# Kernel tuning notes

Hardware: AMD Instinct MI355X
Metric: run time of the kernel (lower is better)

Reference implementation:

```python
import jax, jax.numpy as jnp
import numpy as np

HEADS = 16
HEAD_DIM = 64
DIM = 1024
INNER = HEADS * HEAD_DIM
EPS = 1e-5


def setup_inputs() -> dict:
    key = jax.random.key(0)
    k_x, k_qkv, k_out, k_b = jax.random.split(key, 4)
    B, L = 2, 2048
    x = jax.random.normal(k_x, (B, L, DIM), dtype=jnp.float32)
    # Linear weights stored as [in, out] for x @ W
    w_qkv = jax.random.normal(k_qkv, (DIM, 3 * INNER), dtype=jnp.float32) * (DIM ** -0.5)
    w_out = jax.random.normal(k_out, (INNER, DIM), dtype=jnp.float32) * (INNER ** -0.5)
    b_out = jax.random.normal(k_b, (DIM,), dtype=jnp.float32) * 0.02
    gamma = jnp.ones((DIM,), dtype=jnp.float32)
    beta = jnp.zeros((DIM,), dtype=jnp.float32)
    return {"x": x, "w_qkv": w_qkv, "w_out": w_out, "b_out": b_out, "gamma": gamma, "beta": beta}


def reference(x, w_qkv, w_out, b_out, gamma, beta):
    B, L, C = x.shape
    scale = HEAD_DIM ** -0.5
    qkv = x @ w_qkv  # [B, L, 3*INNER]
    q, k, v = jnp.split(qkv, 3, axis=-1)
    # [B, L, INNER] -> [B, H, L, D]
    def split_heads(t):
        return t.reshape(B, L, HEADS, HEAD_DIM).transpose(0, 2, 1, 3)
    q, k, v = split_heads(q), split_heads(k), split_heads(v)
    dots = jnp.einsum('bhid,bhjd->bhij', q, k) * scale
    attn = jax.nn.softmax(dots, axis=-1)
    out = jnp.einsum('bhij,bhjd->bhid', attn, v)
    out = out.transpose(0, 2, 1, 3).reshape(B, L, INNER)
    out = out @ w_out + b_out
    res = x + out
    mean = jnp.mean(res, axis=-1, keepdims=True)
    var = jnp.var(res, axis=-1, keepdims=True)
    return (res - mean) * jax.lax.rsqrt(var + EPS) * gamma + beta
```

## Files before the change

kernel.cpp:

```cpp
#include <hip/hip_runtime.h>
#include <hip/hip_bf16.h>
#include <stdint.h>

#define HEADS 16
#define HDIM  64
#define DIMC  1024
#define INNER 1024
#define LSEQ  2048
#define BLM   4096

typedef unsigned short u16;
typedef __attribute__((ext_vector_type(8))) short bf16x8;
typedef __attribute__((ext_vector_type(4))) float f32x4;

__device__ __forceinline__ u16 f2bf(float f) {
  union { float f; uint32_t u; } v; v.f = f;
  uint32_t u = v.u;
  return (u16)((u + 0x7fffu + ((u >> 16) & 1u)) >> 16);
}
__device__ __forceinline__ uint32_t pack_bf2(float a, float b) {
  float2 f2; f2.x = a; f2.y = b;
  __hip_bfloat162 t = __float22bfloat162_rn(f2);
  union { __hip_bfloat162 h; uint32_t u; } c; c.h = t; return c.u;
}
__device__ __forceinline__ float fast_exp2(float x) {
  float r; asm("v_exp_f32 %0, %1" : "=v"(r) : "v"(x)); return r;
}

__device__ __forceinline__ void load_lds16(const void* g, void* l) {
  __builtin_amdgcn_global_load_lds(
      (const __attribute__((address_space(1))) uint32_t*)g,
      (__attribute__((address_space(3))) uint32_t*)l, 16, 0, 0);
}

__global__ __launch_bounds__(256) void prep_k(const float* __restrict__ x,
                                              const float* __restrict__ w_qkv,
                                              u16* __restrict__ xb,
                                              u16* __restrict__ wqkvT) {
  __shared__ float tile[32][33];
  int bid = blockIdx.x;
  if (bid < 4096) {
    int i = (bid * 256 + threadIdx.x) * 4;
    float4 v = *(const float4*)(x + i);
    ushort4 o;
    o.x = f2bf(v.x); o.y = f2bf(v.y); o.z = f2bf(v.z); o.w = f2bf(v.w);
    *(ushort4*)(xb + i) = o;
    return;
  }
  int idx = bid - 4096;
  int bx = idx % 96, by = idx / 96;
  int c0 = bx * 32, r0 = by * 32;
  int j = threadIdx.x & 31, i0 = threadIdx.x >> 5;
#pragma unroll
  for (int p = 0; p < 4; ++p) {
    int i = i0 + p * 8;
    tile[i][j] = w_qkv[(size_t)(r0 + i) * 3072 + (c0 + j)];
  }
  __syncthreads();
#pragma unroll
  for (int p = 0; p < 4; ++p) {
    int i = i0 + p * 8;
    wqkvT[(size_t)(c0 + i) * 1024 + (r0 + j)] = f2bf(tile[j][i]);
  }
}

__global__ __launch_bounds__(256) void transpose_cast_k(const float* __restrict__ in,
                                                        u16* __restrict__ out,
                                                        int R, int C) {
  __shared__ float tile[32][33];
  int c0 = blockIdx.x * 32, r0 = blockIdx.y * 32;
  int j = threadIdx.x & 31, i0 = threadIdx.x >> 5;
#pragma unroll
  for (int p = 0; p < 4; ++p) {
    int i = i0 + p * 8;
    tile[i][j] = in[(size_t)(r0 + i) * C + (c0 + j)];
  }
  __syncthreads();
#pragma unroll
  for (int p = 0; p < 4; ++p) {
    int i = i0 + p * 8;
    out[(size_t)(c0 + i) * R + (r0 + j)] = f2bf(tile[j][i]);
  }
}

template <int EPI, int TM>
__global__ __launch_bounds__(256) void gemm_bt(const u16* __restrict__ A,
                                               const u16* __restrict__ Bt,
                                               u16* __restrict__ Cb,
                                               float* __restrict__ Cf,
                                               const float* __restrict__ bias,
                                               const float* __restrict__ resid,
                                               u16* __restrict__ Vt,
                                               int M, int N, int K) {
  constexpr int MI = TM / 32;
  __shared__ alignas(16) u16 As[TM * 64];
  __shared__ alignas(16) u16 Bs[128 * 64];
  const int tid = threadIdx.x;
  const int lane = tid & 63;
  const int w = tid >> 6;
  const int wm = w >> 1, wn = w & 1;
  const int m0 = blockIdx.y * TM, n0 = blockIdx.x * 128;
  const int ln = lane & 15, qq = lane >> 4;
  const f32x4 zero4 = {0.f, 0.f, 0.f, 0.f};

  f32x4 acc[MI][4];
#pragma unroll
  for (int i = 0; i < MI; ++i)
#pragma unroll
    for (int j = 0; j < 4; ++j) acc[i][j] = zero4;

  for (int kt = 0; kt < K; kt += 64) {
    __syncthreads();
#pragma unroll
    for (int p = 0; p < TM / 32; ++p) {
      int t = p * 256 + tid;
      int r = t >> 3;
      int cl = (t & 7) ^ (r & 7);
      load_lds16(A + (size_t)(m0 + r) * K + kt + cl * 8,
                 (char*)As + (p * 256 + w * 64) * 16);
    }
#pragma unroll
    for (int p = 0; p < 4; ++p) {
      int t = p * 256 + tid;
      int r = t >> 3;
      int cl = (t & 7) ^ (r & 7);
      load_lds16(Bt + (size_t)(n0 + r) * K + kt + cl * 8,
                 (char*)Bs + (p * 256 + w * 64) * 16);
    }
    __syncthreads();
#pragma unroll
    for (int ks = 0; ks < 2; ++ks) {
      bf16x8 af[MI], bfr[4];
#pragma unroll
      for (int i = 0; i < MI; ++i) {
        int ra = wm * (TM / 2) + i * 16 + ln;
        af[i] = *(const bf16x8*)(As + (ra * 8 + ((ks * 4 + qq) ^ (ra & 7))) * 8);
      }
#pragma unroll
      for (int j = 0; j < 4; ++j) {
        int rb = wn * 64 + j * 16 + ln;
        bfr[j] = *(const bf16x8*)(Bs + (rb * 8 + ((ks * 4 + qq) ^ (rb & 7))) * 8);
      }
#pragma unroll
      for (int i = 0; i < MI; ++i)
#pragma unroll
        for (int j = 0; j < 4; ++j)
          acc[i][j] = __builtin_amdgcn_mfma_f32_16x16x32_bf16(af[i], bfr[j],
                                                              acc[i][j], 0, 0, 0);
    }
  }

#pragma unroll
  for (int i = 0; i < MI; ++i) {
#pragma unroll
    for (int j = 0; j < 4; ++j) {
      int col = n0 + wn * 64 + j * 16 + ln;
      if (EPI == 1) {
#pragma unroll
        for (int rr = 0; rr < 4; ++rr) {
          int row = m0 + wm * (TM / 2) + i * 16 + qq * 4 + rr;
          Cf[(size_t)row * N + col] =
              acc[i][j][rr] + bias[col] + resid[(size_t)row * N + col];
        }
      } else {
        if (col < 2048) {
#pragma unroll
          for (int rr = 0; rr < 4; ++rr) {
            int row = m0 + wm * (TM / 2) + i * 16 + qq * 4 + rr;
            Cb[(size_t)row * 2048 + col] = f2bf(acc[i][j][rr]);
          }
        } else {
          int dg = col - 2048;
          int hh = dg >> 6, dd = dg & 63;
          int l0 = (m0 & 2047) + wm * (TM / 2) + i * 16 + qq * 4;
          int bb = m0 >> 11;
          ushort4 pk;
          pk.x = f2bf(acc[i][j][0]); pk.y = f2bf(acc[i][j][1]);
          pk.z = f2bf(acc[i][j][2]); pk.w = f2bf(acc[i][j][3]);
          *(ushort4*)(Vt + (((size_t)bb * 16 + hh) * 64 + dd) * 2048 + l0) = pk;
        }
      }
    }
  }
}

__global__ __launch_bounds__(256) void attn_fused(const u16* __restrict__ qk,
                                                  const u16* __restrict__ vt,
                                                  u16* __restrict__ outp) {
  const int bh = blockIdx.x & 31;
  const int qt = blockIdx.x >> 5;
  const int h = bh & 15;
  const int b = bh >> 4;
  const int tid = threadIdx.x;
  const int lane = tid & 63;
  const int w = tid >> 6;
  const int ln = lane & 15, q4 = lane >> 4;
  const int l7 = ln & 7;
  const f32x4 zero4 = {0.f, 0.f, 0.f, 0.f};

  __shared__ alignas(16) u16 Ks[64 * 64];
  __shared__ alignas(16) u16 Vs[64 * 64];
  __shared__ alignas(16) u16 Ps[4][16 * 64];

  const size_t bh_tok = (size_t)b * LSEQ;
  const size_t vbase = ((size_t)b * 16 + h) * 64 * 2048;
  const int baseQ = h * HDIM;

  const float qscale = 0.125f * 1.44269504088896340736f;
  bf16x8 qf[2];
  {
    int row = qt * 64 + w * 16 + ln;
    const u16* p = qk + (bh_tok + row) * 2048 + baseQ;
#pragma unroll
    for (int ks = 0; ks < 2; ++ks) {
      bf16x8 v = *(const bf16x8*)(p + q4 * 8 + 32 * ks);
      bf16x8 o;
#pragma unroll
      for (int jj = 0; jj < 8; ++jj) {
        union { uint32_t u; float f; } cv; cv.u = ((uint32_t)(u16)v[jj]) << 16;
        o[jj] = (short)f2bf(cv.f * qscale);
      }
      qf[ks] = o;
    }
  }

  float lsum = 0.f;
  f32x4 o_acc[4];
#pragma unroll
  for (int dt = 0; dt < 4; ++dt) o_acc[dt] = zero4;

  u16* pw_base = &Ps[w][0];

  for (int jt = 0; jt < 32; ++jt) {
    const int key0 = jt * 64;
    __syncthreads();
#pragma unroll
    for (int iss = 0; iss < 2; ++iss) {
      int idx = iss * 256 + tid;
      int row = idx >> 3, c = idx & 7;
      int cl = c ^ (row & 7);
      load_lds16(qk + (bh_tok + key0 + row) * 2048 + 1024 + baseQ + cl * 8,
                 (char*)Ks + (iss * 256 + w * 64) * 16);
      load_lds16(vt + vbase + (size_t)row * 2048 + key0 + cl * 8,
                 (char*)Vs + (iss * 256 + w * 64) * 16);
    }
    __syncthreads();

    f32x4 S[4];
#pragma unroll
    for (int kt = 0; kt < 4; ++kt) {
      f32x4 a = zero4;
#pragma unroll
      for (int ks = 0; ks < 2; ++ks) {
        bf16x8 kf = *(const bf16x8*)(
            Ks + (((kt * 16 + ln) * 8 + ((ks * 4 + q4) ^ l7)) * 8));
        a = __builtin_amdgcn_mfma_f32_16x16x32_bf16(kf, qf[ks], a, 0, 0, 0);
      }
      S[kt] = a;
    }

#pragma unroll
    for (int kt = 0; kt < 4; ++kt)
#pragma unroll
      for (int r = 0; r < 4; ++r) {
        float p = fast_exp2(S[kt][r]);
        S[kt][r] = p;
        lsum += p;
      }

#pragma unroll
    for (int kt = 0; kt < 4; ++kt) {
      uint2 pd;
      pd.x = pack_bf2(S[kt][0], S[kt][1]);
      pd.y = pack_bf2(S[kt][2], S[kt][3]);
      int u = kt * 2 + (q4 >> 1);
      *(uint2*)(pw_base + ln * 64 + ((u ^ l7) * 8) + (q4 & 1) * 4) = pd;
    }
    asm volatile("s_waitcnt lgkmcnt(0)" ::: "memory");

    bf16x8 pf0 = *(const bf16x8*)(pw_base + ln * 64 + (((0 * 4 + q4) ^ l7) * 8));
    bf16x8 pf1 = *(const bf16x8*)(pw_base + ln * 64 + (((1 * 4 + q4) ^ l7) * 8));

#pragma unroll
    for (int dt = 0; dt < 4; ++dt) {
      bf16x8 va0 = *(const bf16x8*)(
          Vs + (((dt * 16 + ln) * 8 + ((0 * 4 + q4) ^ l7)) * 8));
      o_acc[dt] = __builtin_amdgcn_mfma_f32_16x16x32_bf16(va0, pf0, o_acc[dt], 0, 0, 0);
      bf16x8 va1 = *(const bf16x8*)(
          Vs + (((dt * 16 + ln) * 8 + ((1 * 4 + q4) ^ l7)) * 8));
      o_acc[dt] = __builtin_amdgcn_mfma_f32_16x16x32_bf16(va1, pf1, o_acc[dt], 0, 0, 0);
    }
  }

  lsum += __shfl_xor(lsum, 16);
  lsum += __shfl_xor(lsum, 32);
  float rl = 1.0f / lsum;

  asm volatile("s_waitcnt lgkmcnt(0)" ::: "memory");
#pragma unroll
  for (int dt = 0; dt < 4; ++dt) {
    uint2 pd;
    pd.x = pack_bf2(o_acc[dt][0] * rl, o_acc[dt][1] * rl);
    pd.y = pack_bf2(o_acc[dt][2] * rl, o_acc[dt][3] * rl);
    int u = dt * 2 + (q4 >> 1);
    *(uint2*)(pw_base + ln * 64 + ((u ^ l7) * 8) + (q4 & 1) * 4) = pd;
  }
  asm volatile("s_waitcnt lgkmcnt(0)" ::: "memory");
#pragma unroll
  for (int half = 0; half < 2; ++half) {
    int rr = half * 8 + (lane >> 3);
    int ch = lane & 7;
    bf16x8 rowv = *(const bf16x8*)(pw_base + rr * 64 + ((ch ^ (rr & 7)) * 8));
    int tok = qt * 64 + w * 16 + rr;
    *(bf16x8*)(outp + (bh_tok + tok) * 1024 + baseQ + ch * 8) = rowv;
  }
}

__global__ __launch_bounds__(256) void ln_k(const float* __restrict__ res,
                                            const float* __restrict__ gamma,
                                            const float* __restrict__ beta,
                                            float* __restrict__ out) {
  int w = threadIdx.x >> 6, lane = threadIdx.x & 63;
  int row = blockIdx.x * 4 + w;
  const float* r = res + (size_t)row * DIMC;
  float4 v[4];
  float s = 0.f, ss = 0.f;
#pragma unroll
  for (int p = 0; p < 4; ++p) {
    v[p] = *(const float4*)(r + (p * 64 + lane) * 4);
    s += v[p].x + v[p].y + v[p].z + v[p].w;
    ss += v[p].x * v[p].x + v[p].y * v[p].y + v[p].z * v[p].z + v[p].w * v[p].w;
  }
#pragma unroll
  for (int off = 1; off < 64; off <<= 1) {
    s += __shfl_xor(s, off);
    ss += __shfl_xor(ss, off);
  }
  float mean = s * (1.0f / DIMC);
  float var = ss * (1.0f / DIMC) - mean * mean;
  float inv = rsqrtf(var + 1e-5f);
#pragma unroll
  for (int p = 0; p < 4; ++p) {
    int c = (p * 64 + lane) * 4;
    float4 g = *(const float4*)(gamma + c);
    float4 bt = *(const float4*)(beta + c);
    float4 o;
    o.x = (v[p].x - mean) * inv * g.x + bt.x;
    o.y = (v[p].y - mean) * inv * g.y + bt.y;
    o.z = (v[p].z - mean) * inv * g.z + bt.z;
    o.w = (v[p].w - mean) * inv * g.w + bt.w;
    *(float4*)(out + (size_t)row * DIMC + c) = o;
  }
}

extern "C" void kernel_launch(void* const* d_in, const int* in_sizes, int n_in,
                              void* d_out, int out_size, void* d_ws, size_t ws_size,
                              hipStream_t stream) {
  const float* x = (const float*)d_in[0];
  const float* w_qkv = (const float*)d_in[1];
  const float* w_out = (const float*)d_in[2];
  const float* b_out = (const float*)d_in[3];
  const float* gamma = (const float*)d_in[4];
  const float* beta = (const float*)d_in[5];
  float* outp = (float*)d_out;
  char* ws = (char*)d_ws;

  u16* xb = (u16*)(ws);
  u16* wqkvT = (u16*)(ws + ((size_t)8 << 20));
  u16* qk = (u16*)(ws + ((size_t)14 << 20));
  u16* vt = (u16*)(ws + ((size_t)30 << 20));
  u16* attnout = (u16*)(ws);
  u16* woutT = (u16*)(ws + ((size_t)8 << 20));
  float* res = (float*)(ws + ((size_t)14 << 20));

  prep_k<<<7168, 256, 0, stream>>>(x, w_qkv, xb, wqkvT);
  gemm_bt<2, 128><<<dim3(24, 32), 256, 0, stream>>>(xb, wqkvT, qk, nullptr,
                                                    nullptr, nullptr, vt,
                                                    BLM, 3072, 1024);
  transpose_cast_k<<<dim3(32, 32), 256, 0, stream>>>(w_out, woutT, 1024, 1024);
  attn_fused<<<1024, 256, 0, stream>>>(qk, vt, attnout);
  gemm_bt<1, 64><<<dim3(8, 64), 256, 0, stream>>>(attnout, woutT, nullptr, res,
                                                  b_out, x, nullptr,
                                                  BLM, 1024, 1024);
  ln_k<<<1024, 256, 0, stream>>>(res, gamma, beta, outp);
}
```

Before: 206.2 us.

## Double-buffer K/V tiles and split attention waves over query and key halves

The attention kernel now double-buffers K and V tiles in shared memory, prefetching the next key tile while computing the current one, and uses a single barrier per iteration instead of two. Work is repartitioned so each wave handles 32 query rows against 32 keys of the tile, which reuses each K and V fragment across two query subtiles. The two key-half partial outputs and row sums are combined through shared memory at the end. This adds LDS use, register pressure and a final reduction step in exchange for overlapping global loads with MFMA work and cutting LDS fragment reads.

```diff
diff --git a/kernel.cpp b/kernel.cpp
--- a/kernel.cpp
+++ b/kernel.cpp
@@ -194,125 +194,197 @@
   const int tid = threadIdx.x;
   const int lane = tid & 63;
   const int w = tid >> 6;
+  const int wq = w & 1;
+  const int wk = w >> 1;
   const int ln = lane & 15, q4 = lane >> 4;
   const int l7 = ln & 7;
+  const int swz = (ln >> 1) & 3;
   const f32x4 zero4 = {0.f, 0.f, 0.f, 0.f};
 
-  __shared__ alignas(16) u16 Ks[64 * 64];
-  __shared__ alignas(16) u16 Vs[64 * 64];
-  __shared__ alignas(16) u16 Ps[4][16 * 64];
+  __shared__ alignas(16) char smem[40960];
+  u16* Ksb = (u16*)smem;
+  u16* Vsb = (u16*)(smem + 16384);
+  u16* Psw = (u16*)(smem + 32768);
 
   const size_t bh_tok = (size_t)b * LSEQ;
   const size_t vbase = ((size_t)b * 16 + h) * 64 * 2048;
   const int baseQ = h * HDIM;
 
+  bf16x8 qraw[2][2];
+#pragma unroll
+  for (int nt = 0; nt < 2; ++nt) {
+    int row = qt * 64 + wq * 32 + nt * 16 + ln;
+    const u16* p = qk + (bh_tok + row) * 2048 + baseQ;
+#pragma unroll
+    for (int ks = 0; ks < 2; ++ks)
+      qraw[nt][ks] = *(const bf16x8*)(p + q4 * 8 + 32 * ks);
+  }
+
+#pragma unroll
+  for (int iss = 0; iss < 2; ++iss) {
+    int idx = iss * 256 + tid;
+    int row = idx >> 3, c = idx & 7;
+    int cl = c ^ (row & 7);
+    load_lds16(qk + (bh_tok + row) * 2048 + 1024 + baseQ + cl * 8,
+               (char*)Ksb + (iss * 256 + w * 64) * 16);
+    load_lds16(vt + vbase + (size_t)row * 2048 + cl * 8,
+               (char*)Vsb + (iss * 256 + w * 64) * 16);
+  }
+
   const float qscale = 0.125f * 1.44269504088896340736f;
-  bf16x8 qf[2];
-  {
-    int row = qt * 64 + w * 16 + ln;
-    const u16* p = qk + (bh_tok + row) * 2048 + baseQ;
+  bf16x8 qf[2][2];
+#pragma unroll
+  for (int nt = 0; nt < 2; ++nt)
 #pragma unroll
     for (int ks = 0; ks < 2; ++ks) {
-      bf16x8 v = *(const bf16x8*)(p + q4 * 8 + 32 * ks);
+      bf16x8 v = qraw[nt][ks];
       bf16x8 o;
 #pragma unroll
       for (int jj = 0; jj < 8; ++jj) {
         union { uint32_t u; float f; } cv; cv.u = ((uint32_t)(u16)v[jj]) << 16;
         o[jj] = (short)f2bf(cv.f * qscale);
       }
-      qf[ks] = o;
-    }
-  }
-
-  float lsum = 0.f;
-  f32x4 o_acc[4];
-#pragma unroll
-  for (int dt = 0; dt < 4; ++dt) o_acc[dt] = zero4;
-
-  u16* pw_base = &Ps[w][0];
-
+      qf[nt][ks] = o;
+    }
+
+  float lsum[2] = {0.f, 0.f};
+  f32x4 o_acc[4][2];
+#pragma unroll
+  for (int dt = 0; dt < 4; ++dt) {
+    o_acc[dt][0] = zero4;
+    o_acc[dt][1] = zero4;
+  }
+
+  u16* pw = Psw + w * 1024;
+
+  asm volatile("s_waitcnt vmcnt(0)" ::: "memory");
+  __builtin_amdgcn_s_barrier();
+
+  int cur = 0;
+#pragma unroll 1
   for (int jt = 0; jt < 32; ++jt) {
-    const int key0 = jt * 64;
-    __syncthreads();
-#pragma unroll
-    for (int iss = 0; iss < 2; ++iss) {
-      int idx = iss * 256 + tid;
-      int row = idx >> 3, c = idx & 7;
-      int cl = c ^ (row & 7);
-      load_lds16(qk + (bh_tok + key0 + row) * 2048 + 1024 + baseQ + cl * 8,
-                 (char*)Ks + (iss * 256 + w * 64) * 16);
-      load_lds16(vt + vbase + (size_t)row * 2048 + key0 + cl * 8,
-                 (char*)Vs + (iss * 256 + w * 64) * 16);
-    }
-    __syncthreads();
-
-    f32x4 S[4];
-#pragma unroll
-    for (int kt = 0; kt < 4; ++kt) {
-      f32x4 a = zero4;
+    if (jt < 31) {
+      const int key0 = (jt + 1) * 64;
+#pragma unroll
+      for (int iss = 0; iss < 2; ++iss) {
+        int idx = iss * 256 + tid;
+        int row = idx >> 3, c = idx & 7;
+        int cl = c ^ (row & 7);
+        load_lds16(qk + (bh_tok + key0 + row) * 2048 + 1024 + baseQ + cl * 8,
+                   (char*)Ksb + (cur ^ 1) * 8192 + (iss * 256 + w * 64) * 16);
+        load_lds16(vt + vbase + (size_t)row * 2048 + key0 + cl * 8,
+                   (char*)Vsb + (cur ^ 1) * 8192 + (iss * 256 + w * 64) * 16);
+      }
+    }
+
+    const u16* Ks = Ksb + cur * 4096;
+    const u16* Vs = Vsb + cur * 4096;
+
+    f32x4 s_[2][2];
+#pragma unroll
+    for (int kt = 0; kt < 2; ++kt) { s_[kt][0] = zero4; s_[kt][1] = zero4; }
+#pragma unroll
+    for (int kt = 0; kt < 2; ++kt) {
+      int row = wk * 32 + kt * 16 + ln;
 #pragma unroll
       for (int ks = 0; ks < 2; ++ks) {
-        bf16x8 kf = *(const bf16x8*)(
-            Ks + (((kt * 16 + ln) * 8 + ((ks * 4 + q4) ^ l7)) * 8));
-        a = __builtin_amdgcn_mfma_f32_16x16x32_bf16(kf, qf[ks], a, 0, 0, 0);
-      }
-      S[kt] = a;
-    }
-
-#pragma unroll
-    for (int kt = 0; kt < 4; ++kt)
-#pragma unroll
-      for (int r = 0; r < 4; ++r) {
-        float p = fast_exp2(S[kt][r]);
-        S[kt][r] = p;
-        lsum += p;
-      }
-
-#pragma unroll
-    for (int kt = 0; kt < 4; ++kt) {
-      uint2 pd;
-      pd.x = pack_bf2(S[kt][0], S[kt][1]);
-      pd.y = pack_bf2(S[kt][2], S[kt][3]);
-      int u = kt * 2 + (q4 >> 1);
-      *(uint2*)(pw_base + ln * 64 + ((u ^ l7) * 8) + (q4 & 1) * 4) = pd;
-    }
+        bf16x8 kf = *(const bf16x8*)(Ks + (row * 8 + ((ks * 4 + q4) ^ l7)) * 8);
+        s_[kt][0] = __builtin_amdgcn_mfma_f32_16x16x32_bf16(kf, qf[0][ks], s_[kt][0], 0, 0, 0);
+        s_[kt][1] = __builtin_amdgcn_mfma_f32_16x16x32_bf16(kf, qf[1][ks], s_[kt][1], 0, 0, 0);
+      }
+    }
+
+#pragma unroll
+    for (int kt = 0; kt < 2; ++kt)
+#pragma unroll
+      for (int nt = 0; nt < 2; ++nt)
+#pragma unroll
+        for (int r = 0; r < 4; ++r) {
+          float p = fast_exp2(s_[kt][nt][r]);
+          s_[kt][nt][r] = p;
+          lsum[nt] += p;
+        }
+
+#pragma unroll
+    for (int kt = 0; kt < 2; ++kt)
+#pragma unroll
+      for (int nt = 0; nt < 2; ++nt) {
+        uint2 pd;
+        pd.x = pack_bf2(s_[kt][nt][0], s_[kt][nt][1]);
+        pd.y = pack_bf2(s_[kt][nt][2], s_[kt][nt][3]);
+        int u = (2 * kt + (q4 >> 1)) ^ swz;
+        *(uint2*)(pw + (nt * 16 + ln) * 32 + u * 8 + (q4 & 1) * 4) = pd;
+      }
     asm volatile("s_waitcnt lgkmcnt(0)" ::: "memory");
 
-    bf16x8 pf0 = *(const bf16x8*)(pw_base + ln * 64 + (((0 * 4 + q4) ^ l7) * 8));
-    bf16x8 pf1 = *(const bf16x8*)(pw_base + ln * 64 + (((1 * 4 + q4) ^ l7) * 8));
+    bf16x8 pfrag[2];
+#pragma unroll
+    for (int nt = 0; nt < 2; ++nt)
+      pfrag[nt] = *(const bf16x8*)(pw + (nt * 16 + ln) * 32 + ((q4 ^ swz) * 8));
 
 #pragma unroll
     for (int dt = 0; dt < 4; ++dt) {
-      bf16x8 va0 = *(const bf16x8*)(
-          Vs + (((dt * 16 + ln) * 8 + ((0 * 4 + q4) ^ l7)) * 8));
-      o_acc[dt] = __builtin_amdgcn_mfma_f32_16x16x32_bf16(va0, pf0, o_acc[dt], 0, 0, 0);
-      bf16x8 va1 = *(const bf16x8*)(
-          Vs + (((dt * 16 + ln) * 8 + ((1 * 4 + q4) ^ l7)) * 8));
-      o_acc[dt] = __builtin_amdgcn_mfma_f32_16x16x32_bf16(va1, pf1, o_acc[dt], 0, 0, 0);
-    }
-  }
-
-  lsum += __shfl_xor(lsum, 16);
-  lsum += __shfl_xor(lsum, 32);
-  float rl = 1.0f / lsum;
-
-  asm volatile("s_waitcnt lgkmcnt(0)" ::: "memory");
-#pragma unroll
-  for (int dt = 0; dt < 4; ++dt) {
-    uint2 pd;
-    pd.x = pack_bf2(o_acc[dt][0] * rl, o_acc[dt][1] * rl);
-    pd.y = pack_bf2(o_acc[dt][2] * rl, o_acc[dt][3] * rl);
-    int u = dt * 2 + (q4 >> 1);
-    *(uint2*)(pw_base + ln * 64 + ((u ^ l7) * 8) + (q4 & 1) * 4) = pd;
-  }
-  asm volatile("s_waitcnt lgkmcnt(0)" ::: "memory");
-#pragma unroll
-  for (int half = 0; half < 2; ++half) {
-    int rr = half * 8 + (lane >> 3);
-    int ch = lane & 7;
-    bf16x8 rowv = *(const bf16x8*)(pw_base + rr * 64 + ((ch ^ (rr & 7)) * 8));
-    int tok = qt * 64 + w * 16 + rr;
-    *(bf16x8*)(outp + (bh_tok + tok) * 1024 + baseQ + ch * 8) = rowv;
+      int row = dt * 16 + ln;
+      bf16x8 va = *(const bf16x8*)(Vs + (row * 8 + ((wk * 4 + q4) ^ l7)) * 8);
+      o_acc[dt][0] = __builtin_amdgcn_mfma_f32_16x16x32_bf16(va, pfrag[0], o_acc[dt][0], 0, 0, 0);
+      o_acc[dt][1] = __builtin_amdgcn_mfma_f32_16x16x32_bf16(va, pfrag[1], o_acc[dt][1], 0, 0, 0);
+    }
+
+    asm volatile("s_waitcnt vmcnt(0)" ::: "memory");
+    __builtin_amdgcn_s_barrier();
+    cur ^= 1;
+  }
+
+#pragma unroll
+  for (int nt = 0; nt < 2; ++nt) {
+    lsum[nt] += __shfl_xor(lsum[nt], 16);
+    lsum[nt] += __shfl_xor(lsum[nt], 32);
+  }
+
+  float* osc = (float*)smem;
+  float* lsb = (float*)(smem + 17408);
+  u16* obuf = (u16*)(smem + 17920);
+
+  if (q4 == 0) {
+    lsb[(wq * 2 + wk) * 32 + ln] = lsum[0];
+    lsb[(wq * 2 + wk) * 32 + 16 + ln] = lsum[1];
+  }
+  if (wk == 1) {
+#pragma unroll
+    for (int dt = 0; dt < 4; ++dt)
+#pragma unroll
+      for (int nt = 0; nt < 2; ++nt)
+        *(f32x4*)(osc + (wq * 32 + nt * 16 + ln) * 68 + dt * 16 + q4 * 4) =
+            o_acc[dt][nt];
+  }
+  __syncthreads();
+
+  if (wk == 0) {
+    float rl[2];
+#pragma unroll
+    for (int nt = 0; nt < 2; ++nt)
+      rl[nt] = 1.0f / (lsum[nt] + lsb[(wq * 2 + 1) * 32 + nt * 16 + ln]);
+#pragma unroll
+    for (int dt = 0; dt < 4; ++dt)
+#pragma unroll
+      for (int nt = 0; nt < 2; ++nt) {
+        f32x4 part = *(const f32x4*)(osc + (wq * 32 + nt * 16 + ln) * 68 +
+                                     dt * 16 + q4 * 4);
+        f32x4 o = o_acc[dt][nt] + part;
+        ushort4 pk4;
+        pk4.x = f2bf(o[0] * rl[nt]); pk4.y = f2bf(o[1] * rl[nt]);
+        pk4.z = f2bf(o[2] * rl[nt]); pk4.w = f2bf(o[3] * rl[nt]);
+        *(ushort4*)(obuf + (wq * 32 + nt * 16 + ln) * 72 + dt * 16 + q4 * 4) = pk4;
+      }
+    asm volatile("s_waitcnt lgkmcnt(0)" ::: "memory");
+#pragma unroll
+    for (int it = 0; it < 4; ++it) {
+      int rr = it * 8 + (lane >> 3);
+      int ch = lane & 7;
+      bf16x8 rowv = *(const bf16x8*)(obuf + (wq * 32 + rr) * 72 + ch * 8);
+      int tok = qt * 64 + wq * 32 + rr;
+      *(bf16x8*)(outp + (bh_tok + tok) * 1024 + baseQ + ch * 8) = rowv;
+    }
   }
 }
 
```

Measured after the change: 196.5 us. 1.05x faster.
